# Kernel optimization log

Hardware: AMD Instinct MI355X
Metric: run time of the kernel (lower is better)

## Reference

```python
import jax, jax.numpy as jnp
import numpy as np

D_MODEL = 1024
D_FF = 4096
N_HEADS = 16
HEAD_DIM = D_MODEL // N_HEADS
EPS = 1e-6
B, S = 4, 2048


def _linear_params(key, d_in, d_out):
    kw, kb = jax.random.split(key)
    scale = 1.0 / np.sqrt(d_in)
    w = jax.random.uniform(kw, (d_in, d_out), minval=-scale, maxval=scale, dtype=jnp.float32)
    b = jax.random.uniform(kb, (d_out,), minval=-scale, maxval=scale, dtype=jnp.float32)
    return w, b


def setup_inputs() -> dict:
    key = jax.random.key(0)
    ks = jax.random.split(key, 16)
    x = jax.random.normal(ks[0], (B, S, D_MODEL), dtype=jnp.float32)
    enc = jax.random.normal(ks[1], (B, S, D_MODEL), dtype=jnp.float32)
    # masked self-attention params
    wq1, bq1 = _linear_params(ks[2], D_MODEL, D_MODEL)
    wk1, bk1 = _linear_params(ks[3], D_MODEL, D_MODEL)
    wv1, bv1 = _linear_params(ks[4], D_MODEL, D_MODEL)
    wo1, bo1 = _linear_params(ks[5], D_MODEL, D_MODEL)
    # cross-attention params
    wq2, bq2 = _linear_params(ks[6], D_MODEL, D_MODEL)
    wk2, bk2 = _linear_params(ks[7], D_MODEL, D_MODEL)
    wv2, bv2 = _linear_params(ks[8], D_MODEL, D_MODEL)
    wo2, bo2 = _linear_params(ks[9], D_MODEL, D_MODEL)
    # feed-forward params
    wf1, bf1 = _linear_params(ks[10], D_MODEL, D_FF)
    wf2, bf2 = _linear_params(ks[11], D_FF, D_MODEL)
    # layer norms
    g1 = jnp.ones((D_MODEL,), jnp.float32); be1 = jnp.zeros((D_MODEL,), jnp.float32)
    g2 = jnp.ones((D_MODEL,), jnp.float32); be2 = jnp.zeros((D_MODEL,), jnp.float32)
    g3 = jnp.ones((D_MODEL,), jnp.float32); be3 = jnp.zeros((D_MODEL,), jnp.float32)
    return dict(x=x, encoder_output=enc,
                wq1=wq1, bq1=bq1, wk1=wk1, bk1=bk1, wv1=wv1, bv1=bv1, wo1=wo1, bo1=bo1,
                wq2=wq2, bq2=bq2, wk2=wk2, bk2=bk2, wv2=wv2, bv2=bv2, wo2=wo2, bo2=bo2,
                wf1=wf1, bf1=bf1, wf2=wf2, bf2=bf2,
                g1=g1, be1=be1, g2=g2, be2=be2, g3=g3, be3=be3)


def _layer_norm(x, g, b):
    mu = jnp.mean(x, axis=-1, keepdims=True)
    var = jnp.mean(jnp.square(x - mu), axis=-1, keepdims=True)
    return (x - mu) * jax.lax.rsqrt(var + EPS) * g + b


def _mha(q_in, k_in, v_in, wq, bq, wk, bk, wv, bv, wo, bo, causal):
    b, s, _ = q_in.shape
    q = (q_in @ wq + bq).reshape(b, s, N_HEADS, HEAD_DIM)
    k = (k_in @ wk + bk).reshape(b, -1, N_HEADS, HEAD_DIM)
    v = (v_in @ wv + bv).reshape(b, -1, N_HEADS, HEAD_DIM)
    scores = jnp.einsum('bqhd,bkhd->bhqk', q, k) / np.sqrt(HEAD_DIM)
    if causal:
        mask = jnp.tril(jnp.ones((s, s), dtype=bool))
        scores = jnp.where(mask, scores, jnp.finfo(scores.dtype).min)
    attn = jax.nn.softmax(scores, axis=-1)
    out = jnp.einsum('bhqk,bkhd->bqhd', attn, v).reshape(b, s, D_MODEL)
    return out @ wo + bo


def reference(x, encoder_output,
              wq1, bq1, wk1, bk1, wv1, bv1, wo1, bo1,
              wq2, bq2, wk2, bk2, wv2, bv2, wo2, bo2,
              wf1, bf1, wf2, bf2,
              g1, be1, g2, be2, g3, be3):
    # masked self-attention + residual + LN
    residual = x
    x = _mha(x, x, x, wq1, bq1, wk1, bk1, wv1, bv1, wo1, bo1, causal=True)
    x = _layer_norm(x + residual, g1, be1)
    # cross-attention (note: q=enc, k=enc, v=x as in the original) + residual + LN
    residual = x
    x = _mha(encoder_output, encoder_output, x, wq2, bq2, wk2, bk2, wv2, bv2, wo2, bo2, causal=False)
    x = _layer_norm(x + residual, g2, be2)
    # feed-forward (dropout=0 -> identity in eval) + residual + LN
    residual = x
    x = jax.nn.relu(x @ wf1 + bf1) @ wf2 + bf2
    x = _layer_norm(x + residual, g3, be3)
    return x
```

## Files before the change

### kernel.cpp

```cpp
#include <hip/hip_runtime.h>


typedef _Float16 f16;
typedef _Float16 f16x8 __attribute__((ext_vector_type(8)));
typedef _Float16 f16x4 __attribute__((ext_vector_type(4)));
typedef __fp16 fp16x2 __attribute__((ext_vector_type(2)));
typedef float f32x4 __attribute__((ext_vector_type(4)));
typedef float f32x16 __attribute__((ext_vector_type(16)));
typedef unsigned int u32;

#define AS1 __attribute__((address_space(1)))
#define AS3 __attribute__((address_space(3)))

constexpr int S_LEN = 2048;
constexpr int DM    = 1024;

constexpr long OFF_W    = 0;
constexpr long OFF_XB   = 32L  << 20;
constexpr long OFF_ENC  = 48L  << 20;
constexpr long OFF_Q    = 64L  << 20;
constexpr long OFF_K    = 80L  << 20;
constexpr long OFF_V    = 96L  << 20;
constexpr long OFF_VT   = 112L << 20;
constexpr long OFF_AC   = 128L << 20;
constexpr long OFF_HID  = 144L << 20;
constexpr long OFF_F1   = 208L << 20;
constexpr long OFF_F2   = 240L << 20;
constexpr long OFF_F3   = 272L << 20;
constexpr long OFF_PART = 304L << 20;
constexpr long BUF_BYTES = 336L << 20;

__device__ alignas(4096) unsigned char g_buf[BUF_BYTES];

constexpr long WQ1T = OFF_W + (0L  << 20);
constexpr long WF1T = OFF_W + (16L << 20);
constexpr long WF2T = OFF_W + (24L << 20);
constexpr long WO1T = OFF_W + (6L  << 20);
constexpr long WQ2T = OFF_W + (8L  << 20);
constexpr long WV2T = OFF_W + (12L << 20);
constexpr long WO2T = OFF_W + (14L << 20);

__global__ __launch_bounds__(256) void cvt2_k(const float* __restrict__ x,
                                              const float* __restrict__ enc)
{
    const int bid = blockIdx.x;
    const bool second = bid >= 8192;
    const float* in = second ? enc : x;
    f16* out = (f16*)(g_buf + (second ? OFF_ENC : OFF_XB));
    long i = (long)(second ? bid - 8192 : bid) * 256 + threadIdx.x;
    float4 v = ((const float4*)in)[i];
    f16x4 h;
    h.x = (f16)v.x; h.y = (f16)v.y; h.z = (f16)v.z; h.w = (f16)v.w;
    *(f16x4*)(out + i * 4) = h;
}

struct TWJobs { const float* src[10]; };

__global__ __launch_bounds__(256) void transw_all_k(TWJobs jobs)
{
    __shared__ float t[32][33];
    const int bid = blockIdx.x;
    int j, local;
    if (bid < 8192)       { j = bid >> 10; local = bid & 1023; }
    else if (bid < 12288) { j = 8; local = bid - 8192; }
    else                  { j = 9; local = bid - 12288; }
    const int K = (j == 9) ? 4096 : 1024;
    const int N = (j == 8) ? 4096 : 1024;
    const int tnx = N >> 5;
    const int tx32 = local % tnx, ty32 = local / tnx;
    const long dstOff = (j < 8) ? (long)j * (2L << 20) : ((j == 8) ? WF1T : WF2T);
    const float* W = jobs.src[j];
    f16* Wt = (f16*)(g_buf + dstOff);

    int tx = threadIdx.x, ty = threadIdx.y;
    int c0 = tx32 * 32, r0 = ty32 * 32;
#pragma unroll
    for (int i = 0; i < 4; ++i)
        t[ty + 8*i][tx] = W[(long)(r0 + ty + 8*i) * N + c0 + tx];
    __syncthreads();
#pragma unroll
    for (int i = 0; i < 4; ++i)
        Wt[(long)(c0 + ty + 8*i) * K + r0 + tx] = (f16)t[tx][ty + 8*i];
}

template<int MODE>
__global__ __launch_bounds__(256) void gemm3_k(
    long aOff, long bOff, long cOff, long vtOff,
    const float* __restrict__ b0, const float* __restrict__ b1,
    const float* __restrict__ b2, const float* __restrict__ b3,
    int K, int lda, int ldb, int ldc, long chunkStride, int tvch)
{
    __shared__ alignas(16) f16 As[3][128 * 32];
    __shared__ alignas(16) f16 Bs[3][128 * 32];

    const int tid  = threadIdx.x;
    const int lane = tid & 63;
    const int w    = tid >> 6;
    const int cB   = lane & 15;
    const int hi   = lane >> 4;

    const int nwg = gridDim.x * gridDim.y;
    const int id  = blockIdx.y * gridDim.x + blockIdx.x;
    const int swz = (id & 7) * (nwg >> 3) + (id >> 3);
    const int bx  = swz % gridDim.x, by = swz / gridDim.x;
    const int row0 = by * 128, col0 = bx * 128;

    const f16* Ab = (const f16*)(g_buf + aOff);
    const f16* Bb = (const f16*)(g_buf + bOff);

    const int wr = (w >> 1) * 64;
    const int wc = (w & 1) * 64;

    f32x4 acc[4][4] = {};

    auto stage = [&](int buf, int kt) {
        const int kB = kt * 32;
        const int base = w * 64;
#pragma unroll
        for (int r = 0; r < 2; ++r) {
            const int idx  = r * 256 + base + lane;
            const int srow = idx >> 2, sb = idx & 3;
            const int gk = (sb ^ ((srow >> 1) & 3)) << 3;
            __builtin_amdgcn_global_load_lds(
                (const AS1 void*)(Ab + (long)(row0 + srow) * lda + kB + gk),
                (AS3 void*)(&As[buf][(r * 256 + base) * 8]), 16, 0, 0);
            __builtin_amdgcn_global_load_lds(
                (const AS1 void*)(Bb + (long)(col0 + srow) * ldb + kB + gk),
                (AS3 void*)(&Bs[buf][(r * 256 + base) * 8]), 16, 0, 0);
        }
    };

    const int nt = K >> 5;
    stage(0, 0);
    stage(1, 1);

    for (int t = 0; t < nt; ++t) {
        if (nt - t >= 2) asm volatile("s_waitcnt vmcnt(4)" ::: "memory");
        else             asm volatile("s_waitcnt vmcnt(0)" ::: "memory");
        __builtin_amdgcn_s_barrier();
        __builtin_amdgcn_sched_barrier(0);
        if (t + 2 < nt) stage((t + 2) % 3, t + 2);

        const int cur = t % 3;
        f16x8 af[4], bf[4];
#pragma unroll
        for (int m = 0; m < 4; ++m) {
            const int row = wr + m * 16 + cB;
            af[m] = *(const f16x8*)&As[cur][row * 32 + ((hi ^ ((row >> 1) & 3)) << 3)];
        }
#pragma unroll
        for (int n = 0; n < 4; ++n) {
            const int row = wc + n * 16 + cB;
            bf[n] = *(const f16x8*)&Bs[cur][row * 32 + ((hi ^ ((row >> 1) & 3)) << 3)];
        }
        __builtin_amdgcn_s_setprio(1);
#pragma unroll
        for (int m = 0; m < 4; ++m)
#pragma unroll
            for (int n = 0; n < 4; ++n)
                acc[m][n] = __builtin_amdgcn_mfma_f32_16x16x32_f16(af[m], bf[n], acc[m][n], 0, 0, 0);
        __builtin_amdgcn_s_setprio(0);
    }

    const int ch = col0 >> 10;
    const float* bp = (ch == 0) ? b0 : (ch == 1) ? b1 : (ch == 2) ? b2 : b3;

    if (MODE == 0 && ch == tvch) {
        f16* Vt = (f16*)(g_buf + vtOff);
#pragma unroll
        for (int m = 0; m < 4; ++m) {
#pragma unroll
            for (int n = 0; n < 4; ++n) {
                const int c = col0 + wc + n * 16 + cB;
                const int hh = (c >> 6) & 15, dd = c & 63;
                const float bv = bp[c & 1023];
                const int r0e = row0 + wr + m * 16 + hi * 4;
                const int bb = r0e >> 11, sS = r0e & 2047;
                f16x4 hv;
#pragma unroll
                for (int jj = 0; jj < 4; ++jj) hv[jj] = (f16)(acc[m][n][jj] + bv);
                *(f16x4*)(Vt + (((long)(bb * 16 + hh) * 64 + dd) * 2048 + sS)) = hv;
            }
        }
        return;
    }

    float* Cf = (float*)(g_buf + cOff);
    f16*  Ch = (f16*)(g_buf + cOff);
    const long cBase = (long)ch * chunkStride;
#pragma unroll
    for (int m = 0; m < 4; ++m) {
#pragma unroll
        for (int n = 0; n < 4; ++n) {
            const int c = col0 + wc + n * 16 + cB;
            const float bv = bp[c & 1023];
#pragma unroll
            for (int jj = 0; jj < 4; ++jj) {
                const int r = row0 + wr + m * 16 + hi * 4 + jj;
                float v = acc[m][n][jj] + bv;
                const long idx = cBase + (long)r * ldc + (c & 1023);
                if constexpr (MODE == 2) Cf[idx] = v;
                else                     Ch[idx] = (f16)v;
            }
        }
    }
}

template<int MODE>
__global__ __launch_bounds__(256, 2) void gemm4_k(
    long aOff, long bOff, long cOff, long partOff, long vtOff,
    const float* __restrict__ b0, const float* __restrict__ b1,
    const float* __restrict__ b2, const float* __restrict__ b3,
    int K, int lda, int ldb, int ldc, long chunkStride, int tvch)
{
    __shared__ alignas(16) f16 As[3][128 * 32];
    __shared__ alignas(16) f16 Bs[3][256 * 32];

    const int tid  = threadIdx.x;
    const int lane = tid & 63;
    const int w    = tid >> 6;
    const int cB   = lane & 15;
    const int hi   = lane >> 4;

    const int gx = gridDim.x, gy = gridDim.y;
    const int nwg = gx * gy * gridDim.z;
    const int id  = ((int)blockIdx.z * gy + (int)blockIdx.y) * gx + (int)blockIdx.x;
    const int swz = (id & 7) * (nwg >> 3) + (id >> 3);
    const int bx  = swz % gx;
    const int rem = swz / gx;
    const int by  = rem % gy;
    const int bz  = rem / gy;
    const int row0 = by * 128, col0 = bx * 256;

    const f16* Ab = (const f16*)(g_buf + aOff) + (long)bz * K;
    const f16* Bb = (const f16*)(g_buf + bOff) + (long)bz * K;

    const int wr = (w >> 1) * 64;
    const int wc = (w & 1) * 128;

    f32x4 acc[4][8] = {};

    auto stage = [&](int buf, int kt) {
        const int kB = kt * 32;
        const int base = w * 64;
#pragma unroll
        for (int r = 0; r < 2; ++r) {
            const int idx  = r * 256 + base + lane;
            const int srow = idx >> 2, sb = idx & 3;
            const int gk = (sb ^ ((srow >> 1) & 3)) << 3;
            __builtin_amdgcn_global_load_lds(
                (const AS1 void*)(Ab + (long)(row0 + srow) * lda + kB + gk),
                (AS3 void*)(&As[buf][(r * 256 + base) * 8]), 16, 0, 0);
        }
#pragma unroll
        for (int r = 0; r < 4; ++r) {
            const int idx  = r * 256 + base + lane;
            const int srow = idx >> 2, sb = idx & 3;
            const int gk = (sb ^ ((srow >> 1) & 3)) << 3;
            __builtin_amdgcn_global_load_lds(
                (const AS1 void*)(Bb + (long)(col0 + srow) * ldb + kB + gk),
                (AS3 void*)(&Bs[buf][(r * 256 + base) * 8]), 16, 0, 0);
        }
    };

    const int nt = K >> 5;
    stage(0, 0);
    stage(1, 1);

    for (int t = 0; t < nt; ++t) {
        if (nt - t >= 2) asm volatile("s_waitcnt vmcnt(6)" ::: "memory");
        else             asm volatile("s_waitcnt vmcnt(0)" ::: "memory");
        __builtin_amdgcn_s_barrier();
        __builtin_amdgcn_sched_barrier(0);
        if (t + 2 < nt) stage((t + 2) % 3, t + 2);

        const int cur = t % 3;
        f16x8 af[4], bf[8];
#pragma unroll
        for (int m = 0; m < 4; ++m) {
            const int row = wr + m * 16 + cB;
            af[m] = *(const f16x8*)&As[cur][row * 32 + ((hi ^ ((row >> 1) & 3)) << 3)];
        }
#pragma unroll
        for (int n = 0; n < 8; ++n) {
            const int row = wc + n * 16 + cB;
            bf[n] = *(const f16x8*)&Bs[cur][row * 32 + ((hi ^ ((row >> 1) & 3)) << 3)];
        }
        __builtin_amdgcn_s_setprio(1);
#pragma unroll
        for (int m = 0; m < 4; ++m)
#pragma unroll
            for (int n = 0; n < 8; ++n)
                acc[m][n] = __builtin_amdgcn_mfma_f32_16x16x32_f16(af[m], bf[n], acc[m][n], 0, 0, 0);
        __builtin_amdgcn_s_setprio(0);
    }

    const int ch = col0 >> 10;
    const float* bp = (ch == 0) ? b0 : (ch == 1) ? b1 : (ch == 2) ? b2 : b3;

    if (MODE == 0 && ch == tvch) {
        f16* Vt = (f16*)(g_buf + vtOff);
#pragma unroll
        for (int m = 0; m < 4; ++m) {
#pragma unroll
            for (int n = 0; n < 8; ++n) {
                const int c = col0 + wc + n * 16 + cB;
                const int hh = (c >> 6) & 15, dd = c & 63;
                const float bv = bp[c & 1023];
                const int r0e = row0 + wr + m * 16 + hi * 4;
                const int bb = r0e >> 11, sS = r0e & 2047;
                f16x4 hv;
#pragma unroll
                for (int jj = 0; jj < 4; ++jj) hv[jj] = (f16)(acc[m][n][jj] + bv);
                *(f16x4*)(Vt + (((long)(bb * 16 + hh) * 64 + dd) * 2048 + sS)) = hv;
            }
        }
        return;
    }

    float* Cf = (float*)(g_buf + (bz ? partOff : cOff));
    f16*  Ch = (f16*)(g_buf + cOff);
    const long cBase = (long)ch * chunkStride;
#pragma unroll
    for (int m = 0; m < 4; ++m) {
#pragma unroll
        for (int n = 0; n < 8; ++n) {
            const int c = col0 + wc + n * 16 + cB;
            const float bv = bz ? 0.f : bp[c & 1023];
#pragma unroll
            for (int jj = 0; jj < 4; ++jj) {
                const int r = row0 + wr + m * 16 + hi * 4 + jj;
                float v = acc[m][n][jj] + bv;
                if constexpr (MODE == 1) v = fmaxf(v, 0.f);
                const long idx = cBase + (long)r * ldc + (c & 1023);
                if constexpr (MODE == 2) Cf[idx] = v;
                else                     Ch[idx] = (f16)v;
            }
        }
    }
}

template<int CAUSAL>
__global__ __launch_bounds__(256, 4) void flash_k(long qOff, long kOff, long vtOff, long oOff)
{
    __shared__ alignas(16) f16 KV[2][2][4096];

    const int tid  = threadIdx.x;
    const int lane = tid & 63;
    const int w    = tid >> 6;
    const int ql   = lane & 31;
    const int s    = lane >> 5;

    const int raw   = (int)blockIdx.y * (int)gridDim.x + (int)blockIdx.x;
    const int newid = (raw & 7) * 128 + (raw >> 3);
    const int bh    = newid >> 4;
    int qt = newid & 15;
    if (CAUSAL) qt = 15 - qt;

    const int b = bh >> 4, h = bh & 15;
    const int q0 = qt * 128;
    const long tokB = (long)b * S_LEN;

    const f16* Qb  = (const f16*)(g_buf + qOff);
    const f16* Kb  = (const f16*)(g_buf + kOff);
    const f16* Vtb = (const f16*)(g_buf + vtOff) + (long)bh * 64 * S_LEN;
    f16* Ob = (f16*)(g_buf + oOff);

    const int r8 = lane >> 3;
    const int c8 = lane & 7;
    const int sb = c8 ^ r8;
    const int nch = CAUSAL ? 2 * (qt + 1) : (S_LEN / 64);

    auto stage = [&](int buf, int c) {
        const int kv0s = c * 64;
#pragma unroll
        for (int t = 0; t < 2; ++t) {
            const int grp = w * 2 + t;
            const int row = grp * 8 + r8;
            __builtin_amdgcn_global_load_lds(
                (const AS1 void*)(Kb + (tokB + kv0s + row) * DM + h * 64 + sb * 8),
                (AS3 void*)(&KV[buf][0][grp * 512]), 16, 0, 0);
            __builtin_amdgcn_global_load_lds(
                (const AS1 void*)(Vtb + (long)row * S_LEN + kv0s + sb * 8),
                (AS3 void*)(&KV[buf][1][grp * 512]), 16, 0, 0);
        }
    };

    stage(0, 0);

    f16x8 qf[4];
    {
        const f16 hs = (f16)(0.125f * 1.44269504088896f);
        const f16* qrow = Qb + (tokB + q0 + w * 32 + ql) * DM + h * 64 + s * 8;
#pragma unroll
        for (int kk = 0; kk < 4; ++kk) {
            qf[kk] = *(const f16x8*)(qrow + kk * 16);
#pragma unroll
            for (int i = 0; i < 8; ++i) qf[kk][i] = qf[kk][i] * hs;
        }
    }

    f32x16 oacc[2] = {};
    float mrow = -1e30f, lrow = 0.f;

    for (int c = 0; c < nch; ++c) {
        const int cur = c & 1;
        const int kv0 = c * 64;

        asm volatile("s_waitcnt vmcnt(0) lgkmcnt(0)" ::: "memory");
        __builtin_amdgcn_sched_barrier(0);
        __builtin_amdgcn_s_barrier();
        __builtin_amdgcn_sched_barrier(0);
        if (c + 1 < nch) stage(cur ^ 1, c + 1);

        const bool active = !CAUSAL || (kv0 <= q0 + w * 32 + 31);
        if (active) {
            f32x16 p[2] = {};
            __builtin_amdgcn_s_setprio(1);
#pragma unroll
            for (int kk = 0; kk < 4; ++kk) {
                const int t16 = (kk * 2 + s) ^ (ql & 7);
                f16x8 kf0 = *(const f16x8*)((const char*)&KV[cur][0][0] + ql * 128 + t16 * 16);
                f16x8 kf1 = *(const f16x8*)((const char*)&KV[cur][0][0] + (32 + ql) * 128 + t16 * 16);
                p[0] = __builtin_amdgcn_mfma_f32_32x32x16_f16(kf0, qf[kk], p[0], 0, 0, 0);
                p[1] = __builtin_amdgcn_mfma_f32_32x32x16_f16(kf1, qf[kk], p[1], 0, 0, 0);
            }
            __builtin_amdgcn_s_setprio(0);

            if (CAUSAL && (kv0 + 63 > q0 + w * 32)) {
                const int q = q0 + w * 32 + ql;
#pragma unroll
                for (int v = 0; v < 2; ++v)
#pragma unroll
                    for (int r = 0; r < 16; ++r) {
                        const int kv = kv0 + v * 32 + (r & 3) + 8 * (r >> 2) + 4 * s;
                        if (kv > q) p[v][r] = -1e30f;
                    }
            }

            float rmax = fmaxf(p[0][0], p[0][1]);
#pragma unroll
            for (int r = 2; r < 16; r += 2) rmax = fmaxf(fmaxf(p[0][r], p[0][r + 1]), rmax);
#pragma unroll
            for (int r = 0; r < 16; r += 2) rmax = fmaxf(fmaxf(p[1][r], p[1][r + 1]), rmax);
            rmax = fmaxf(rmax, __shfl_xor(rmax, 32));

            if (!__all(rmax <= mrow + 8.0f)) {
                const float mn = fmaxf(mrow, rmax);
                const float alpha = __builtin_amdgcn_exp2f(mrow - mn);
                lrow *= alpha;
                mrow = mn;
#pragma unroll
                for (int r = 0; r < 16; ++r) {
                    const int qr = (r & 3) + 8 * (r >> 2) + 4 * s;
                    const float ab = __shfl(alpha, qr);
                    oacc[0][r] *= ab;
                    oacc[1][r] *= ab;
                }
            }

            u32 pk[2][4][2];
            float rsum = 0.f;
#pragma unroll
            for (int v = 0; v < 2; ++v)
#pragma unroll
                for (int a = 0; a < 4; ++a)
#pragma unroll
                    for (int cc = 0; cc < 2; ++cc) {
                        const float e0 = __builtin_amdgcn_exp2f(p[v][4 * a + 2 * cc] - mrow);
                        const float e1 = __builtin_amdgcn_exp2f(p[v][4 * a + 2 * cc + 1] - mrow);
                        rsum += e0 + e1;
                        union { fp16x2 h; u32 u; } cv;
                        cv.h = __builtin_amdgcn_cvt_pkrtz(e0, e1);
                        pk[v][a][cc] = cv.u;
                    }
            rsum += __shfl_xor(rsum, 32);
            lrow += rsum;

            u32 loc[2][2][2], exv[2][2][2];
#pragma unroll
            for (int v = 0; v < 2; ++v)
#pragma unroll
                for (int k1 = 0; k1 < 2; ++k1)
#pragma unroll
                    for (int cc = 0; cc < 2; ++cc) {
                        const u32 pe = pk[v][2 * k1][cc];
                        const u32 po = pk[v][2 * k1 + 1][cc];
                        loc[v][k1][cc] = s ? po : pe;
                        const u32 snd = s ? pe : po;
                        exv[v][k1][cc] = (u32)__shfl_xor((int)snd, 32);
                    }

            __builtin_amdgcn_s_setprio(1);
#pragma unroll
            for (int ks = 0; ks < 4; ++ks) {
                const int v = ks >> 1, k1 = ks & 1;
                union { u32 u[4]; f16x8 hv; } pa;
                pa.u[0] = s ? exv[v][k1][0] : loc[v][k1][0];
                pa.u[1] = s ? exv[v][k1][1] : loc[v][k1][1];
                pa.u[2] = s ? loc[v][k1][0] : exv[v][k1][0];
                pa.u[3] = s ? loc[v][k1][1] : exv[v][k1][1];
                const int tv = (ks * 2 + s) ^ (ql & 7);
                f16x8 vf0 = *(const f16x8*)((const char*)&KV[cur][1][0] + ql * 128 + tv * 16);
                f16x8 vf1 = *(const f16x8*)((const char*)&KV[cur][1][0] + (32 + ql) * 128 + tv * 16);
                oacc[0] = __builtin_amdgcn_mfma_f32_32x32x16_f16(pa.hv, vf0, oacc[0], 0, 0, 0);
                oacc[1] = __builtin_amdgcn_mfma_f32_32x32x16_f16(pa.hv, vf1, oacc[1], 0, 0, 0);
            }
            __builtin_amdgcn_s_setprio(0);
        }
    }

    asm volatile("s_waitcnt lgkmcnt(0)" ::: "memory");
    __builtin_amdgcn_sched_barrier(0);
    __builtin_amdgcn_s_barrier();

    f16* Es = ((f16*)&KV[0][0][0]) + w * 2304;
    const float linv = 1.0f / lrow;
#pragma unroll
    for (int r = 0; r < 16; ++r) {
        const int qr = (r & 3) + 8 * (r >> 2) + 4 * s;
        const float lb = __shfl(linv, qr);
        Es[qr * 72 + ql]      = (f16)(oacc[0][r] * lb);
        Es[qr * 72 + 32 + ql] = (f16)(oacc[1][r] * lb);
    }
    const int orow = lane >> 1;
    const int oh   = (lane & 1) * 32;
    const f16* srcp = ((const f16*)&KV[0][0][0]) + w * 2304 + orow * 72 + oh;
    f16* dst = Ob + (tokB + q0 + w * 32 + orow) * DM + h * 64 + oh;
#pragma unroll
    for (int t = 0; t < 4; ++t)
        *(f16x8*)(dst + t * 8) = *(const f16x8*)(srcp + t * 8);
}

__global__ __launch_bounds__(256) void ln_k(
    long inOff, long in2Off, const float* __restrict__ residExt, long residOff,
    const float* __restrict__ gamma, const float* __restrict__ beta,
    float* __restrict__ outFExt, long outFOff, long outHOff)
{
    const float* in    = (const float*)(g_buf + inOff);
    const float* resid = residExt ? residExt : (const float*)(g_buf + residOff);
    float* outF = outFExt ? outFExt : (float*)(g_buf + outFOff);
    f16*  outH = (f16*)(g_buf + outHOff);

    const long row = blockIdx.x;
    const int tid = threadIdx.x;
    const int lane = tid & 63, wid = tid >> 6;

    float4 a  = ((const float4*)(in    + row * DM))[tid];
    float4 rr = ((const float4*)(resid + row * DM))[tid];
    float x0 = a.x + rr.x, x1 = a.y + rr.y, x2 = a.z + rr.z, x3 = a.w + rr.w;
    if (in2Off >= 0) {
        const float* in2 = (const float*)(g_buf + in2Off);
        float4 p = ((const float4*)(in2 + row * DM))[tid];
        x0 += p.x; x1 += p.y; x2 += p.z; x3 += p.w;
    }

    __shared__ float red[4];
    float ss = x0 + x1 + x2 + x3;
#pragma unroll
    for (int o = 32; o > 0; o >>= 1) ss += __shfl_xor(ss, o);
    if (lane == 0) red[wid] = ss;
    __syncthreads();
    const float mu = (red[0] + red[1] + red[2] + red[3]) * (1.0f / DM);

    float d0 = x0 - mu, d1 = x1 - mu, d2 = x2 - mu, d3 = x3 - mu;
    float qq = d0*d0 + d1*d1 + d2*d2 + d3*d3;
#pragma unroll
    for (int o = 32; o > 0; o >>= 1) qq += __shfl_xor(qq, o);
    __syncthreads();
    if (lane == 0) red[wid] = qq;
    __syncthreads();
    const float var = (red[0] + red[1] + red[2] + red[3]) * (1.0f / DM);
    const float rs = rsqrtf(var + 1e-6f);

    float4 g  = ((const float4*)gamma)[tid];
    float4 be = ((const float4*)beta)[tid];
    float y0 = d0 * rs * g.x + be.x;
    float y1 = d1 * rs * g.y + be.y;
    float y2 = d2 * rs * g.z + be.z;
    float y3 = d3 * rs * g.w + be.w;

    ((float4*)(outF + row * DM))[tid] = make_float4(y0, y1, y2, y3);
    f16x4 hh; hh.x = (f16)y0; hh.y = (f16)y1; hh.z = (f16)y2; hh.w = (f16)y3;
    *(f16x4*)(outH + row * DM + tid * 4) = hh;
}

extern "C" void kernel_launch(void* const* d_in, const int* in_sizes, int n_in,
                              void* d_out, int out_size, void* d_ws, size_t ws_size,
                              hipStream_t stream)
{
    (void)in_sizes; (void)n_in; (void)d_ws; (void)ws_size; (void)out_size;
    const float* x   = (const float*)d_in[0];
    const float* enc = (const float*)d_in[1];
    const float* wq1 = (const float*)d_in[2];  const float* bq1 = (const float*)d_in[3];
    const float* wk1 = (const float*)d_in[4];  const float* bk1 = (const float*)d_in[5];
    const float* wv1 = (const float*)d_in[6];  const float* bv1 = (const float*)d_in[7];
    const float* wo1 = (const float*)d_in[8];  const float* bo1 = (const float*)d_in[9];
    const float* wq2 = (const float*)d_in[10]; const float* bq2 = (const float*)d_in[11];
    const float* wk2 = (const float*)d_in[12]; const float* bk2 = (const float*)d_in[13];
    const float* wv2 = (const float*)d_in[14]; const float* bv2 = (const float*)d_in[15];
    const float* wo2 = (const float*)d_in[16]; const float* bo2 = (const float*)d_in[17];
    const float* wf1 = (const float*)d_in[18]; const float* bf1 = (const float*)d_in[19];
    const float* wf2 = (const float*)d_in[20]; const float* bf2 = (const float*)d_in[21];
    const float* g1  = (const float*)d_in[22]; const float* be1 = (const float*)d_in[23];
    const float* g2  = (const float*)d_in[24]; const float* be2 = (const float*)d_in[25];
    const float* g3  = (const float*)d_in[26]; const float* be3 = (const float*)d_in[27];
    float* out = (float*)d_out;

    const dim3 T256(256), T32x8(32, 8);
    const long QKV_CHUNK = 8192L * 1024;

    cvt2_k<<<16384, T256, 0, stream>>>(x, enc);
    TWJobs jobs;
    jobs.src[0] = wq1; jobs.src[1] = wk1; jobs.src[2] = wv1; jobs.src[3] = wo1;
    jobs.src[4] = wq2; jobs.src[5] = wk2; jobs.src[6] = wv2; jobs.src[7] = wo2;
    jobs.src[8] = wf1; jobs.src[9] = wf2;
    transw_all_k<<<16384, T32x8, 0, stream>>>(jobs);

    gemm4_k<0><<<dim3(12, 64, 1), T256, 0, stream>>>(OFF_XB, WQ1T, OFF_Q, 0, OFF_VT,
        bq1, bk1, bv1, bv1, 1024, 1024, 1024, 1024, QKV_CHUNK, 2);
    flash_k<1><<<dim3(16, 64), T256, 0, stream>>>(OFF_Q, OFF_K, OFF_VT, OFF_AC);
    gemm3_k<2><<<dim3(8, 64), T256, 0, stream>>>(OFF_AC, WO1T, OFF_F2, 0,
        bo1, bo1, bo1, bo1, 1024, 1024, 1024, 1024, 1024, -1);
    ln_k<<<8192, T256, 0, stream>>>(OFF_F2, -1, x, 0, g1, be1, nullptr, OFF_F1, OFF_XB);

    gemm4_k<0><<<dim3(8, 64, 1), T256, 0, stream>>>(OFF_ENC, WQ2T, OFF_Q, 0, 0,
        bq2, bk2, bk2, bk2, 1024, 1024, 1024, 1024, QKV_CHUNK, -1);
    gemm3_k<0><<<dim3(8, 64), T256, 0, stream>>>(OFF_XB, WV2T, OFF_V, OFF_VT,
        bv2, bv2, bv2, bv2, 1024, 1024, 1024, 1024, 1024, 0);
    flash_k<0><<<dim3(16, 64), T256, 0, stream>>>(OFF_Q, OFF_K, OFF_VT, OFF_AC);
    gemm3_k<2><<<dim3(8, 64), T256, 0, stream>>>(OFF_AC, WO2T, OFF_F2, 0,
        bo2, bo2, bo2, bo2, 1024, 1024, 1024, 1024, 1024, -1);
    ln_k<<<8192, T256, 0, stream>>>(OFF_F2, -1, nullptr, OFF_F1, g2, be2, nullptr, OFF_F3, OFF_XB);

    gemm4_k<1><<<dim3(16, 64, 1), T256, 0, stream>>>(OFF_XB, WF1T, OFF_HID, 0, 0,
        bf1, bf1 + 1024, bf1 + 2048, bf1 + 3072, 1024, 1024, 1024, 4096, 1024, -1);
    gemm4_k<2><<<dim3(4, 64, 2), T256, 0, stream>>>(OFF_HID, WF2T, OFF_F2, OFF_PART, 0,
        bf2, bf2, bf2, bf2, 2048, 4096, 4096, 1024, 1024, -1);
    ln_k<<<8192, T256, 0, stream>>>(OFF_F2, OFF_PART, nullptr, OFF_F3, g3, be3, out, 0, OFF_XB);
}
```

Measured before the change: 672.4 us.

## Replace 128x256 GEMM with 256x256 8-wave kernel and interleaved plane prefetch

Swaps the 256-thread 128x256-tile GEMM for a 512-thread 256x256-tile kernel with K=64 steps. Each step is split into four half-planes, and the next step's A/B planes are prefetched between MFMA phases into a double buffer. The larger tile raises operand reuse and arithmetic intensity per LDS byte. In exchange it halves the block count, which risks wave-quantization and occupancy loss on 256 CUs, and it adds more barriers per K step.

```diff
diff --git a/kernel.cpp b/kernel.cpp
--- a/kernel.cpp
+++ b/kernel.cpp
@@ -207,14 +207,14 @@
 }
 
 template<int MODE>
-__global__ __launch_bounds__(256, 2) void gemm4_k(
+__global__ __launch_bounds__(512, 1) void gemm8_k(
     long aOff, long bOff, long cOff, long partOff, long vtOff,
     const float* __restrict__ b0, const float* __restrict__ b1,
     const float* __restrict__ b2, const float* __restrict__ b3,
     int K, int lda, int ldb, int ldc, long chunkStride, int tvch)
 {
-    __shared__ alignas(16) f16 As[3][128 * 32];
-    __shared__ alignas(16) f16 Bs[3][256 * 32];
+    __shared__ alignas(16) f16 As[2][2][8192];
+    __shared__ alignas(16) f16 Bs[2][2][8192];
 
     const int tid  = threadIdx.x;
     const int lane = tid & 63;
@@ -230,68 +230,118 @@
     const int rem = swz / gx;
     const int by  = rem % gy;
     const int bz  = rem / gy;
-    const int row0 = by * 128, col0 = bx * 256;
+    const int row0 = by * 256, col0 = bx * 256;
 
     const f16* Ab = (const f16*)(g_buf + aOff) + (long)bz * K;
     const f16* Bb = (const f16*)(g_buf + bOff) + (long)bz * K;
 
-    const int wr = (w >> 1) * 64;
-    const int wc = (w & 1) * 128;
-
-    f32x4 acc[4][8] = {};
-
-    auto stage = [&](int buf, int kt) {
-        const int kB = kt * 32;
-        const int base = w * 64;
+    const int wr = (w >> 2) * 128;
+    const int wc = (w & 3) * 64;
+
+    f32x4 acc[8][4] = {};
+
+    auto stagePlane = [&](int buf, int kt, int mat, int kh) {
+        const int kB = kt * 64 + kh * 32;
+        const f16* src = mat ? Bb : Ab;
+        const int ld   = mat ? ldb : lda;
+        const int r0g  = mat ? col0 : row0;
+        f16* dst = mat ? &Bs[buf][kh][0] : &As[buf][kh][0];
 #pragma unroll
         for (int r = 0; r < 2; ++r) {
-            const int idx  = r * 256 + base + lane;
+            const int idx  = r * 512 + w * 64 + lane;
             const int srow = idx >> 2, sb = idx & 3;
             const int gk = (sb ^ ((srow >> 1) & 3)) << 3;
             __builtin_amdgcn_global_load_lds(
-                (const AS1 void*)(Ab + (long)(row0 + srow) * lda + kB + gk),
-                (AS3 void*)(&As[buf][(r * 256 + base) * 8]), 16, 0, 0);
-        }
-#pragma unroll
-        for (int r = 0; r < 4; ++r) {
-            const int idx  = r * 256 + base + lane;
-            const int srow = idx >> 2, sb = idx & 3;
-            const int gk = (sb ^ ((srow >> 1) & 3)) << 3;
-            __builtin_amdgcn_global_load_lds(
-                (const AS1 void*)(Bb + (long)(col0 + srow) * ldb + kB + gk),
-                (AS3 void*)(&Bs[buf][(r * 256 + base) * 8]), 16, 0, 0);
+                (const AS1 void*)(src + (long)(r0g + srow) * ld + kB + gk),
+                (AS3 void*)(dst + (r * 512 + w * 64) * 8), 16, 0, 0);
         }
     };
 
-    const int nt = K >> 5;
-    stage(0, 0);
-    stage(1, 1);
+    auto rdA = [&](int buf, int kh, int mf) -> f16x8 {
+        const int row = wr + mf * 16 + cB;
+        return *(const f16x8*)&As[buf][kh][row * 32 + ((hi ^ ((row >> 1) & 3)) << 3)];
+    };
+    auto rdB = [&](int buf, int kh, int nf) -> f16x8 {
+        const int row = wc + nf * 16 + cB;
+        return *(const f16x8*)&Bs[buf][kh][row * 32 + ((hi ^ ((row >> 1) & 3)) << 3)];
+    };
+
+    const int nt = K >> 6;
+    stagePlane(0, 0, 0, 0);
+    stagePlane(0, 0, 1, 0);
+    stagePlane(0, 0, 0, 1);
+    stagePlane(0, 0, 1, 1);
 
     for (int t = 0; t < nt; ++t) {
-        if (nt - t >= 2) asm volatile("s_waitcnt vmcnt(6)" ::: "memory");
-        else             asm volatile("s_waitcnt vmcnt(0)" ::: "memory");
+        const int cur = t & 1, nxt = cur ^ 1;
+        const bool pf = (t + 1 < nt);
+        f16x8 a[4], b[4];
+
+        asm volatile("s_waitcnt vmcnt(4)" ::: "memory");
         __builtin_amdgcn_s_barrier();
         __builtin_amdgcn_sched_barrier(0);
-        if (t + 2 < nt) stage((t + 2) % 3, t + 2);
-
-        const int cur = t % 3;
-        f16x8 af[4], bf[8];
-#pragma unroll
-        for (int m = 0; m < 4; ++m) {
-            const int row = wr + m * 16 + cB;
-            af[m] = *(const f16x8*)&As[cur][row * 32 + ((hi ^ ((row >> 1) & 3)) << 3)];
-        }
-#pragma unroll
-        for (int n = 0; n < 8; ++n) {
-            const int row = wc + n * 16 + cB;
-            bf[n] = *(const f16x8*)&Bs[cur][row * 32 + ((hi ^ ((row >> 1) & 3)) << 3)];
-        }
+#pragma unroll
+        for (int n = 0; n < 4; ++n) b[n] = rdB(cur, 0, n);
+#pragma unroll
+        for (int m = 0; m < 4; ++m) a[m] = rdA(cur, 0, m);
+        if (pf) stagePlane(nxt, t + 1, 0, 0);
+        asm volatile("s_waitcnt lgkmcnt(0)" ::: "memory");
+        __builtin_amdgcn_sched_barrier(0);
         __builtin_amdgcn_s_setprio(1);
 #pragma unroll
         for (int m = 0; m < 4; ++m)
 #pragma unroll
-            for (int n = 0; n < 8; ++n)
-                acc[m][n] = __builtin_amdgcn_mfma_f32_16x16x32_f16(af[m], bf[n], acc[m][n], 0, 0, 0);
+            for (int n = 0; n < 4; ++n)
+                acc[m][n] = __builtin_amdgcn_mfma_f32_16x16x32_f16(a[m], b[n], acc[m][n], 0, 0, 0);
+        __builtin_amdgcn_s_setprio(0);
+
+        __builtin_amdgcn_s_barrier();
+        __builtin_amdgcn_sched_barrier(0);
+#pragma unroll
+        for (int m = 0; m < 4; ++m) a[m] = rdA(cur, 0, m + 4);
+        if (pf) stagePlane(nxt, t + 1, 1, 0);
+        asm volatile("s_waitcnt lgkmcnt(0)" ::: "memory");
+        __builtin_amdgcn_sched_barrier(0);
+        __builtin_amdgcn_s_setprio(1);
+#pragma unroll
+        for (int m = 0; m < 4; ++m)
+#pragma unroll
+            for (int n = 0; n < 4; ++n)
+                acc[4 + m][n] = __builtin_amdgcn_mfma_f32_16x16x32_f16(a[m], b[n], acc[4 + m][n], 0, 0, 0);
+        __builtin_amdgcn_s_setprio(0);
+
+        if (pf) asm volatile("s_waitcnt vmcnt(4)" ::: "memory");
+        else    asm volatile("s_waitcnt vmcnt(0)" ::: "memory");
+        __builtin_amdgcn_s_barrier();
+        __builtin_amdgcn_sched_barrier(0);
+#pragma unroll
+        for (int n = 0; n < 4; ++n) b[n] = rdB(cur, 1, n);
+#pragma unroll
+        for (int m = 0; m < 4; ++m) a[m] = rdA(cur, 1, m);
+        if (pf) stagePlane(nxt, t + 1, 0, 1);
+        asm volatile("s_waitcnt lgkmcnt(0)" ::: "memory");
+        __builtin_amdgcn_sched_barrier(0);
+        __builtin_amdgcn_s_setprio(1);
+#pragma unroll
+        for (int m = 0; m < 4; ++m)
+#pragma unroll
+            for (int n = 0; n < 4; ++n)
+                acc[m][n] = __builtin_amdgcn_mfma_f32_16x16x32_f16(a[m], b[n], acc[m][n], 0, 0, 0);
+        __builtin_amdgcn_s_setprio(0);
+
+        __builtin_amdgcn_s_barrier();
+        __builtin_amdgcn_sched_barrier(0);
+#pragma unroll
+        for (int m = 0; m < 4; ++m) a[m] = rdA(cur, 1, m + 4);
+        if (pf) stagePlane(nxt, t + 1, 1, 1);
+        asm volatile("s_waitcnt lgkmcnt(0)" ::: "memory");
+        __builtin_amdgcn_sched_barrier(0);
+        __builtin_amdgcn_s_setprio(1);
+#pragma unroll
+        for (int m = 0; m < 4; ++m)
+#pragma unroll
+            for (int n = 0; n < 4; ++n)
+                acc[4 + m][n] = __builtin_amdgcn_mfma_f32_16x16x32_f16(a[m], b[n], acc[4 + m][n], 0, 0, 0);
         __builtin_amdgcn_s_setprio(0);
     }
 
@@ -301,9 +351,9 @@
     if (MODE == 0 && ch == tvch) {
         f16* Vt = (f16*)(g_buf + vtOff);
 #pragma unroll
-        for (int m = 0; m < 4; ++m) {
-#pragma unroll
-            for (int n = 0; n < 8; ++n) {
+        for (int m = 0; m < 8; ++m) {
+#pragma unroll
+            for (int n = 0; n < 4; ++n) {
                 const int c = col0 + wc + n * 16 + cB;
                 const int hh = (c >> 6) & 15, dd = c & 63;
                 const float bv = bp[c & 1023];
@@ -322,9 +372,9 @@
     f16*  Ch = (f16*)(g_buf + cOff);
     const long cBase = (long)ch * chunkStride;
 #pragma unroll
-    for (int m = 0; m < 4; ++m) {
-#pragma unroll
-        for (int n = 0; n < 8; ++n) {
+    for (int m = 0; m < 8; ++m) {
+#pragma unroll
+        for (int n = 0; n < 4; ++n) {
             const int c = col0 + wc + n * 16 + cB;
             const float bv = bz ? 0.f : bp[c & 1023];
 #pragma unroll
@@ -607,7 +657,7 @@
     const float* g3  = (const float*)d_in[26]; const float* be3 = (const float*)d_in[27];
     float* out = (float*)d_out;
 
-    const dim3 T256(256), T32x8(32, 8);
+    const dim3 T256(256), T512(512), T32x8(32, 8);
     const long QKV_CHUNK = 8192L * 1024;
 
     cvt2_k<<<16384, T256, 0, stream>>>(x, enc);
@@ -617,14 +667,14 @@
     jobs.src[8] = wf1; jobs.src[9] = wf2;
     transw_all_k<<<16384, T32x8, 0, stream>>>(jobs);
 
-    gemm4_k<0><<<dim3(12, 64, 1), T256, 0, stream>>>(OFF_XB, WQ1T, OFF_Q, 0, OFF_VT,
+    gemm8_k<0><<<dim3(12, 32, 1), T512, 0, stream>>>(OFF_XB, WQ1T, OFF_Q, 0, OFF_VT,
         bq1, bk1, bv1, bv1, 1024, 1024, 1024, 1024, QKV_CHUNK, 2);
     flash_k<1><<<dim3(16, 64), T256, 0, stream>>>(OFF_Q, OFF_K, OFF_VT, OFF_AC);
     gemm3_k<2><<<dim3(8, 64), T256, 0, stream>>>(OFF_AC, WO1T, OFF_F2, 0,
         bo1, bo1, bo1, bo1, 1024, 1024, 1024, 1024, 1024, -1);
     ln_k<<<8192, T256, 0, stream>>>(OFF_F2, -1, x, 0, g1, be1, nullptr, OFF_F1, OFF_XB);
 
-    gemm4_k<0><<<dim3(8, 64, 1), T256, 0, stream>>>(OFF_ENC, WQ2T, OFF_Q, 0, 0,
+    gemm8_k<0><<<dim3(8, 32, 1), T512, 0, stream>>>(OFF_ENC, WQ2T, OFF_Q, 0, 0,
         bq2, bk2, bk2, bk2, 1024, 1024, 1024, 1024, QKV_CHUNK, -1);
     gemm3_k<0><<<dim3(8, 64), T256, 0, stream>>>(OFF_XB, WV2T, OFF_V, OFF_VT,
         bv2, bv2, bv2, bv2, 1024, 1024, 1024, 1024, 1024, 0);
@@ -633,9 +683,9 @@
         bo2, bo2, bo2, bo2, 1024, 1024, 1024, 1024, 1024, -1);
     ln_k<<<8192, T256, 0, stream>>>(OFF_F2, -1, nullptr, OFF_F1, g2, be2, nullptr, OFF_F3, OFF_XB);
 
-    gemm4_k<1><<<dim3(16, 64, 1), T256, 0, stream>>>(OFF_XB, WF1T, OFF_HID, 0, 0,
+    gemm8_k<1><<<dim3(16, 32, 1), T512, 0, stream>>>(OFF_XB, WF1T, OFF_HID, 0, 0,
         bf1, bf1 + 1024, bf1 + 2048, bf1 + 3072, 1024, 1024, 1024, 4096, 1024, -1);
-    gemm4_k<2><<<dim3(4, 64, 2), T256, 0, stream>>>(OFF_HID, WF2T, OFF_F2, OFF_PART, 0,
+    gemm8_k<2><<<dim3(4, 32, 2), T512, 0, stream>>>(OFF_HID, WF2T, OFF_F2, OFF_PART, 0,
         bf2, bf2, bf2, bf2, 2048, 4096, 4096, 1024, 1024, -1);
     ln_k<<<8192, T256, 0, stream>>>(OFF_F2, OFF_PART, nullptr, OFF_F3, g3, be3, out, 0, OFF_XB);
 }
```

Result: faster. 643.7 us (-4.3%).
